# Performance work log

Hardware: AMD Instinct MI355X
Metric: run time of the kernel (lower is better)

## Reference

```python
import jax, jax.numpy as jnp
import numpy as np

VOCAB, EMBED, MAXLEN, UNITS, F1, BATCH = 50000, 256, 512, 32, 16, 512

def setup_inputs() -> dict:
    key = jax.random.key(0)
    ks = jax.random.split(key, 9)
    tokens = jax.random.randint(ks[0], (BATCH, MAXLEN), 0, VOCAB, dtype=jnp.int32)
    emb_table = jax.random.normal(ks[1], (VOCAB, EMBED), dtype=jnp.float32) * 0.02
    # SimpleRNN params (Keras: kernel, recurrent_kernel, bias)
    Wx = jax.random.normal(ks[2], (EMBED, UNITS), dtype=jnp.float32) * (1.0 / np.sqrt(EMBED))
    Wh = jax.random.normal(ks[3], (UNITS, UNITS), dtype=jnp.float32) * (1.0 / np.sqrt(UNITS))
    b  = jnp.zeros((UNITS,), dtype=jnp.float32)
    W1 = jax.random.normal(ks[4], (UNITS, F1), dtype=jnp.float32) * (1.0 / np.sqrt(UNITS))
    b1 = jnp.zeros((F1,), dtype=jnp.float32)
    W2 = jax.random.normal(ks[5], (F1, 1), dtype=jnp.float32) * (1.0 / np.sqrt(F1))
    b2 = jnp.zeros((1,), dtype=jnp.float32)
    return {"tokens": tokens, "emb_table": emb_table, "Wx": Wx, "Wh": Wh, "b": b,
            "W1": W1, "b1": b1, "W2": W2, "b2": b2}

def reference(tokens, emb_table, Wx, Wh, b, W1, b1, W2, b2):
    # Embedding lookup: [B, T, E]
    x = emb_table[tokens]
    # SimpleRNN recurrence (tanh), return last hidden state. Dropout disabled (inference).
    xs = jnp.transpose(x, (1, 0, 2))  # time-major [T, B, E]
    h0 = jnp.zeros((tokens.shape[0], Wh.shape[0]), dtype=x.dtype)

    def step(h, x_t):
        h_new = jnp.tanh(x_t @ Wx + h @ Wh + b)
        return h_new, None

    h_last, _ = jax.lax.scan(step, h0, xs)
    # Flatten is a no-op on [B, 32]; Dense heads are linear (no activation), then sigmoid.
    z = (h_last @ W1 + b1) @ W2 + b2
    return jax.nn.sigmoid(z)  # [B, 1]
```

## Files before the change

### kernel.cpp

```cpp
#include <hip/hip_runtime.h>
#include <hip/hip_bf16.h>
#include <math.h>

#define TT 512
#define BB 512
#define EE 256
#define UU 32
#define FF1 16
#define NWAVE 2048

__device__ __forceinline__ float fast_tanh(float x) {
    float e = __builtin_amdgcn_exp2f(x * 2.8853900817779268f);
    float r = __builtin_amdgcn_rcpf(e + 1.0f);
    return fmaf(-2.0f, r, 1.0f);
}

__device__ __forceinline__ float rdlane(float v, int lane) {
    return __int_as_float(__builtin_amdgcn_readlane(__float_as_int(v), lane));
}

#define DPP_ADD(v, ctrl)                                                    \
    (v) += __int_as_float(__builtin_amdgcn_update_dpp(                      \
        0, __float_as_int(v), (ctrl), 0xf, 0xf, true))

__global__ __launch_bounds__(64) void proj_dpp(
    const float* __restrict__ emb, const float* __restrict__ Wx,
    const float* __restrict__ bias, float* __restrict__ P, int nrows)
{
    const int L = threadIdx.x;
    const int g = L >> 4;
    const int c = L & 15;
    const int wv = blockIdx.x;

    float w[16][8];
    #pragma unroll
    for (int kk = 0; kk < 16; ++kk) {
        const float4* src = (const float4*)(Wx + (size_t)(kk * 16 + c) * UU + g * 8);
        float4 a = src[0], b = src[1];
        w[kk][0] = a.x; w[kk][1] = a.y; w[kk][2] = a.z; w[kk][3] = a.w;
        w[kk][4] = b.x; w[kk][5] = b.y; w[kk][6] = b.z; w[kk][7] = b.w;
    }
    float bs[8];
    #pragma unroll
    for (int uu = 0; uu < 8; ++uu) bs[uu] = bias[g * 8 + uu];

    auto rowptr = [&](int i) {
        int r = wv + NWAVE * i;
        if (r >= nrows) r = nrows - 1;
        return emb + (size_t)r * EE;
    };

    float xA[16], xB[16];
    {
        const float* rp = rowptr(0);
        #pragma unroll
        for (int kk = 0; kk < 16; ++kk) xA[kk] = rp[kk * 16 + c];
    }

    const int NI = (nrows - 1 - wv) / NWAVE + 1;

    for (int i = 0; i < NI; ++i) {
        {
            const float* rp = rowptr(i + 1 < NI ? i + 1 : i);
            #pragma unroll
            for (int kk = 0; kk < 16; ++kk) xB[kk] = rp[kk * 16 + c];
        }

        float p[8];
        #pragma unroll
        for (int uu = 0; uu < 8; ++uu) p[uu] = 0.f;
        #pragma unroll
        for (int kk = 0; kk < 16; ++kk) {
            const float xk = xA[kk];
            #pragma unroll
            for (int uu = 0; uu < 8; ++uu)
                p[uu] = fmaf(xk, w[kk][uu], p[uu]);
        }

        #pragma unroll
        for (int uu = 0; uu < 8; ++uu) {
            DPP_ADD(p[uu], 0x111);
            DPP_ADD(p[uu], 0x112);
            DPP_ADD(p[uu], 0x114);
            DPP_ADD(p[uu], 0x118);
        }

        if (c == 15) {
            const int r = wv + NWAVE * i;
            float4 o0, o1;
            o0.x = p[0] + bs[0]; o0.y = p[1] + bs[1];
            o0.z = p[2] + bs[2]; o0.w = p[3] + bs[3];
            o1.x = p[4] + bs[4]; o1.y = p[5] + bs[5];
            o1.z = p[6] + bs[6]; o1.w = p[7] + bs[7];
            float4* dst = (float4*)(P + (size_t)r * UU + g * 8);
            dst[0] = o0; dst[1] = o1;
        }

        #pragma unroll
        for (int kk = 0; kk < 16; ++kk) xA[kk] = xB[kk];
    }
}

__global__ __launch_bounds__(64) void scan_heads(
    const int* __restrict__ tokens, const float* __restrict__ P,
    const float* __restrict__ Wh,
    const float* __restrict__ W1, const float* __restrict__ b1,
    const float* __restrict__ W2, const float* __restrict__ b2,
    float* __restrict__ out)
{
    __shared__ float xs[TT * UU];

    const int L = threadIdx.x;
    const int u = L & 31;
    const int half16 = (L >> 5) << 4;
    const int b = blockIdx.x;
    const int* trow = tokens + b * TT;

    float wh[16];
    #pragma unroll
    for (int kk = 0; kk < 16; ++kk) wh[kk] = Wh[(half16 + kk) * UU + u];

    int addrA[16];
    #pragma unroll
    for (int kk = 0; kk < 16; ++kk) addrA[kk] = (half16 + kk) << 2;

    const int sub = L >> 3;
    const int q   = L & 7;
    for (int c = 0; c < 8; ++c) {
        int tk8[8];
        #pragma unroll
        for (int i = 0; i < 8; ++i)
            tk8[i] = trow[c * 64 + i * 8 + sub];
        #pragma unroll
        for (int i = 0; i < 8; ++i) {
            const float* src = P + (size_t)tk8[i] * UU + q * 4;
            float* dst = xs + (c * 64 + i * 8) * UU;
            __builtin_amdgcn_global_load_lds(
                (const __attribute__((address_space(1))) void*)src,
                (__attribute__((address_space(3))) void*)dst, 16, 0, 0);
        }
    }
    __syncthreads();

    const bool lower = (L < 32);
    float xr[4];
    #pragma unroll
    for (int j = 0; j < 4; ++j) {
        float xv = xs[j * UU + u];
        xr[j] = lower ? xv : 0.f;
    }

    float h = 0.f;

    for (int t = 0; t < TT; t += 4) {
        #pragma unroll
        for (int j = 0; j < 4; ++j) {
            float xn = xs[((t + 4 + j) & (TT - 1)) * UU + u];
            xn = lower ? xn : 0.f;

            const int hb = __float_as_int(h);
            float v[16];
            #pragma unroll
            for (int kk = 0; kk < 16; ++kk)
                v[kk] = __int_as_float(__builtin_amdgcn_ds_bpermute(addrA[kk], hb));

            float a0 = fmaf(v[0], wh[0], xr[j]);
            float a1 = v[1] * wh[1];
            float a2 = v[2] * wh[2];
            float a3 = v[3] * wh[3];
            #pragma unroll
            for (int kk = 4; kk < 16; kk += 4) {
                a0 = fmaf(v[kk],     wh[kk],     a0);
                a1 = fmaf(v[kk + 1], wh[kk + 1], a1);
                a2 = fmaf(v[kk + 2], wh[kk + 2], a2);
                a3 = fmaf(v[kk + 3], wh[kk + 3], a3);
            }
            float sh = (a0 + a1) + (a2 + a3);

            float tot;
#if __has_builtin(__builtin_amdgcn_permlane32_swap)
            {
                auto r = __builtin_amdgcn_permlane32_swap(
                    __float_as_int(sh), __float_as_int(sh), false, false);
                tot = __int_as_float((int)r[0]) + __int_as_float((int)r[1]);
            }
#else
            {
                const int addrX = ((L + 32) & 63) << 2;
                tot = sh + __int_as_float(
                    __builtin_amdgcn_ds_bpermute(addrX, __float_as_int(sh)));
            }
#endif
            h = fast_tanh(tot);
            xr[j] = xn;
        }
    }

    const int j = threadIdx.x & 15;
    float s = b1[j];
    #pragma unroll
    for (int k = 0; k < UU; ++k) {
        float hk = rdlane(h, k);
        s = fmaf(hk, W1[k * FF1 + j], s);
    }
    float z = b2[0];
    #pragma unroll
    for (int jj = 0; jj < FF1; ++jj) {
        float yj = rdlane(s, jj);
        z = fmaf(yj, W2[jj], z);
    }
    if (threadIdx.x == 0) {
        float e = __builtin_amdgcn_exp2f(-z * 1.4426950408889634f);
        out[b] = __builtin_amdgcn_rcpf(1.0f + e);
    }
}

extern "C" void kernel_launch(void* const* d_in, const int* in_sizes, int n_in,
                              void* d_out, int out_size, void* d_ws, size_t ws_size,
                              hipStream_t stream) {
    const int*   tokens = (const int*)  d_in[0];
    const float* emb    = (const float*)d_in[1];
    const float* Wx     = (const float*)d_in[2];
    const float* Wh     = (const float*)d_in[3];
    const float* bias   = (const float*)d_in[4];
    const float* W1     = (const float*)d_in[5];
    const float* b1     = (const float*)d_in[6];
    const float* W2     = (const float*)d_in[7];
    const float* b2     = (const float*)d_in[8];
    float* out = (float*)d_out;

    const int vocab = in_sizes[1] / EE;
    float* P = (float*)d_ws;

    proj_dpp<<<dim3(NWAVE), dim3(64), 0, stream>>>(
        emb, Wx, bias, P, vocab);

    scan_heads<<<dim3(BB), dim3(64), 0, stream>>>(
        tokens, P, Wh, W1, b1, W2, b2, out);
}
```

Before: 206.9 us.

## Use readlane broadcast for recurrence and fold tanh scale into weights

After: 182.7 us. 1.13x faster.

```diff
diff --git a/kernel.cpp b/kernel.cpp
--- a/kernel.cpp
+++ b/kernel.cpp
@@ -9,11 +9,7 @@
 #define FF1 16
 #define NWAVE 2048
 
-__device__ __forceinline__ float fast_tanh(float x) {
-    float e = __builtin_amdgcn_exp2f(x * 2.8853900817779268f);
-    float r = __builtin_amdgcn_rcpf(e + 1.0f);
-    return fmaf(-2.0f, r, 1.0f);
-}
+#define TWO_LOG2E 2.8853900817779268f
 
 __device__ __forceinline__ float rdlane(float v, int lane) {
     return __int_as_float(__builtin_amdgcn_readlane(__float_as_int(v), lane));
@@ -88,10 +84,14 @@
         if (c == 15) {
             const int r = wv + NWAVE * i;
             float4 o0, o1;
-            o0.x = p[0] + bs[0]; o0.y = p[1] + bs[1];
-            o0.z = p[2] + bs[2]; o0.w = p[3] + bs[3];
-            o1.x = p[4] + bs[4]; o1.y = p[5] + bs[5];
-            o1.z = p[6] + bs[6]; o1.w = p[7] + bs[7];
+            o0.x = (p[0] + bs[0]) * TWO_LOG2E;
+            o0.y = (p[1] + bs[1]) * TWO_LOG2E;
+            o0.z = (p[2] + bs[2]) * TWO_LOG2E;
+            o0.w = (p[3] + bs[3]) * TWO_LOG2E;
+            o1.x = (p[4] + bs[4]) * TWO_LOG2E;
+            o1.y = (p[5] + bs[5]) * TWO_LOG2E;
+            o1.z = (p[6] + bs[6]) * TWO_LOG2E;
+            o1.w = (p[7] + bs[7]) * TWO_LOG2E;
             float4* dst = (float4*)(P + (size_t)r * UU + g * 8);
             dst[0] = o0; dst[1] = o1;
         }
@@ -112,17 +112,12 @@
 
     const int L = threadIdx.x;
     const int u = L & 31;
-    const int half16 = (L >> 5) << 4;
     const int b = blockIdx.x;
     const int* trow = tokens + b * TT;
 
-    float wh[16];
-    #pragma unroll
-    for (int kk = 0; kk < 16; ++kk) wh[kk] = Wh[(half16 + kk) * UU + u];
-
-    int addrA[16];
-    #pragma unroll
-    for (int kk = 0; kk < 16; ++kk) addrA[kk] = (half16 + kk) << 2;
+    float wh[UU];
+    #pragma unroll
+    for (int k = 0; k < UU; ++k) wh[k] = Wh[k * UU + u] * TWO_LOG2E;
 
     const int sub = L >> 3;
     const int q   = L & 7;
@@ -142,58 +137,42 @@
     }
     __syncthreads();
 
-    const bool lower = (L < 32);
-    float xr[4];
-    #pragma unroll
-    for (int j = 0; j < 4; ++j) {
-        float xv = xs[j * UU + u];
-        xr[j] = lower ? xv : 0.f;
-    }
+    float xr[8];
+    #pragma unroll
+    for (int j = 0; j < 8; ++j) xr[j] = xs[j * UU + u];
 
     float h = 0.f;
 
-    for (int t = 0; t < TT; t += 4) {
-        #pragma unroll
-        for (int j = 0; j < 4; ++j) {
-            float xn = xs[((t + 4 + j) & (TT - 1)) * UU + u];
-            xn = lower ? xn : 0.f;
-
-            const int hb = __float_as_int(h);
-            float v[16];
-            #pragma unroll
-            for (int kk = 0; kk < 16; ++kk)
-                v[kk] = __int_as_float(__builtin_amdgcn_ds_bpermute(addrA[kk], hb));
-
-            float a0 = fmaf(v[0], wh[0], xr[j]);
-            float a1 = v[1] * wh[1];
-            float a2 = v[2] * wh[2];
-            float a3 = v[3] * wh[3];
-            #pragma unroll
-            for (int kk = 4; kk < 16; kk += 4) {
-                a0 = fmaf(v[kk],     wh[kk],     a0);
-                a1 = fmaf(v[kk + 1], wh[kk + 1], a1);
-                a2 = fmaf(v[kk + 2], wh[kk + 2], a2);
-                a3 = fmaf(v[kk + 3], wh[kk + 3], a3);
+    for (int t = 0; t < TT; t += 8) {
+        float xn[8];
+        #pragma unroll
+        for (int j = 0; j < 8; ++j)
+            xn[j] = xs[((t + 8 + j) & (TT - 1)) * UU + u];
+
+        #pragma unroll
+        for (int j = 0; j < 8; ++j) {
+            float hv[UU];
+            #pragma unroll
+            for (int k = 0; k < UU; ++k) hv[k] = rdlane(h, k);
+
+            float a0 = fmaf(hv[0], wh[0], xr[j]);
+            float a1 = hv[1] * wh[1];
+            float a2 = hv[2] * wh[2];
+            float a3 = hv[3] * wh[3];
+            #pragma unroll
+            for (int k = 4; k < UU; k += 4) {
+                a0 = fmaf(hv[k],     wh[k],     a0);
+                a1 = fmaf(hv[k + 1], wh[k + 1], a1);
+                a2 = fmaf(hv[k + 2], wh[k + 2], a2);
+                a3 = fmaf(hv[k + 3], wh[k + 3], a3);
             }
-            float sh = (a0 + a1) + (a2 + a3);
-
-            float tot;
-#if __has_builtin(__builtin_amdgcn_permlane32_swap)
-            {
-                auto r = __builtin_amdgcn_permlane32_swap(
-                    __float_as_int(sh), __float_as_int(sh), false, false);
-                tot = __int_as_float((int)r[0]) + __int_as_float((int)r[1]);
-            }
-#else
-            {
-                const int addrX = ((L + 32) & 63) << 2;
-                tot = sh + __int_as_float(
-                    __builtin_amdgcn_ds_bpermute(addrX, __float_as_int(sh)));
-            }
-#endif
-            h = fast_tanh(tot);
-            xr[j] = xn;
-        }
+            float e = __builtin_amdgcn_exp2f((a0 + a1) + (a2 + a3));
+            float r = __builtin_amdgcn_rcpf(e + 1.0f);
+            h = fmaf(-2.0f, r, 1.0f);
+        }
+
+        #pragma unroll
+        for (int j = 0; j < 8; ++j) xr[j] = xn[j];
     }
 
     const int j = threadIdx.x & 15;
```
